# Performance work log

Measured on AMD Instinct MI355X. Metric: run time of the kernel, lower is better.

The kernel has to match this reference:

```python
import jax, jax.numpy as jnp
from jax import lax
import numpy as np

N, H, W, E, B = 4096, 7, 18, 16384, 64
NCONV = 3

def _conv2d(x, w, b=None):
    y = lax.conv_general_dilated(x, w, (1, 1), 'SAME', dimension_numbers=('NCHW', 'OIHW', 'NCHW'))
    return y if b is None else y + b[None, :, None, None]

def _bn(x, g, b):
    # training-mode batchnorm over (batch, H, W) per channel
    m = x.mean(axis=(0, 2, 3), keepdims=True)
    v = x.var(axis=(0, 2, 3), keepdims=True)
    return g[None, :, None, None] * (x - m) * lax.rsqrt(v + 1e-5) + b[None, :, None, None]

def _conv_layer(atom, es, et, nw, ew, lw, lb, bg, bb):
    # gather edge features (E,16,H,W); FastEdgeNetwork zip truncates to ONE iteration
    z = _conv2d(atom[et], ew)
    th = _conv2d(atom, nw)[es]
    z = jax.nn.elu(th * z)
    h = _conv2d(z, lw, lb)                      # (E,32,H,W)
    filt, core = jnp.split(h, 2, axis=1)
    msg = jax.nn.sigmoid(filt) * jax.nn.softplus(core)
    out = atom.at[es].add(msg)                  # scatter-add aggregation
    return atom + _bn(out, bg, bb)              # bn + residual


def setup_inputs() -> dict:
    key = jax.random.key(0)
    ks = iter(jax.random.split(key, 64))
    def rn(shape, s=0.05):
        return jax.random.normal(next(ks), shape, dtype=jnp.float32) * s
    d = {}
    d['nodes'] = jax.random.normal(next(ks), (N, H, W), dtype=jnp.float32)
    d['edge_sources'] = jax.random.randint(next(ks), (E,), 0, N)
    d['edge_targets'] = jax.random.randint(next(ks), (E,), 0, N)
    d['graph_indices'] = jnp.arange(N, dtype=jnp.int32) // (N // B)
    d['node_counts'] = jnp.full((B,), N // B, dtype=jnp.int32)
    d['nsites'] = jax.random.randint(next(ks), (B,), 1, 50)
    d['spacegroups'] = jax.random.randint(next(ks), (B,), 1, 231)
    d['emb_w'] = rn((16, 1, 3, 3)); d['emb_b'] = jnp.zeros((16,))
    d['cl_node_w'] = rn((NCONV, 16, 16, 3, 3)); d['cl_edge_w'] = rn((NCONV, 16, 16, 3, 3))
    d['cl_lin_w'] = rn((NCONV, 32, 16, 3, 3)); d['cl_lin_b'] = jnp.zeros((NCONV, 32))
    d['cl_bn_g'] = jnp.ones((NCONV, 16)); d['cl_bn_b'] = jnp.zeros((NCONV, 16))
    d['se_w1'] = rn((16, 2)); d['se_b1'] = jnp.zeros((16,))
    d['se_w2'] = rn((16, 2)); d['se_b2'] = jnp.zeros((16,))
    d['se_conv_w'] = rn((16, 1, 3, 3)); d['se_conv_b'] = jnp.zeros((16,))
    d['se_bn_g'] = jnp.ones((16,)); d['se_bn_b'] = jnp.zeros((16,))
    d['sf_conv_w'] = rn((16, 16, 3, 3)); d['sf_conv_b'] = jnp.zeros((16,))
    d['sf_bn_g'] = jnp.ones((16,)); d['sf_bn_b'] = jnp.zeros((16,))
    d['ctf_w'] = rn((16, 16, 3, 3)); d['ctf_b'] = jnp.zeros((16,))
    d['fc1_w'] = rn((32, 16 * H * W)); d['fc1_b'] = jnp.zeros((32,))
    d['fc2_w'] = rn((32, 32)); d['fc2_b'] = jnp.zeros((32,))
    d['reg_w'] = rn((1, 32)); d['reg_b'] = jnp.zeros((1,))
    d['fc3_w'] = rn((1, 144)); d['fc3_b'] = jnp.zeros((1,))
    d['eps'] = jnp.full((1,), 0.1, dtype=jnp.float32)
    return d


def reference(nodes, edge_sources, edge_targets, graph_indices, node_counts, nsites, spacegroups,
              emb_w, emb_b, cl_node_w, cl_edge_w, cl_lin_w, cl_lin_b, cl_bn_g, cl_bn_b,
              se_w1, se_b1, se_w2, se_b2, se_conv_w, se_conv_b, se_bn_g, se_bn_b,
              sf_conv_w, sf_conv_b, sf_bn_g, sf_bn_b, ctf_w, ctf_b,
              fc1_w, fc1_b, fc2_w, fc2_b, reg_w, reg_b, fc3_w, fc3_b, eps):
    sp = jax.nn.softplus
    # atom embedding: (N,1,7,18) -> (N,16,7,18)
    atom = sp(_conv2d(nodes[:, None], emb_w, emb_b))
    for l in range(NCONV):
        atom = _conv_layer(atom, edge_sources, edge_targets, cl_node_w[l], cl_edge_w[l],
                           cl_lin_w[l], cl_lin_b[l], cl_bn_g[l], cl_bn_b[l])
    # space branch: outer product of two 16-d embeddings of (nsites, spacegroup)
    so = jnp.stack([nsites, spacegroups], axis=1).astype(jnp.float32)    # (B,2)
    row = so @ se_w1.T + se_b1
    col = so @ se_w2.T + se_b2
    outer = (row[:, :, None] * col[:, None, :])[:, None]                 # (B,1,16,16)
    semb = sp(_bn(_conv2d(outer, se_conv_w, se_conv_b), se_bn_g, se_bn_b))  # (B,16,16,16)
    y = _bn(_conv2d(semb, sf_conv_w, sf_conv_b), sf_bn_g, sf_bn_b)
    y = lax.reduce_window(y, -jnp.inf, lax.max, (1, 1, 5, 5), (1, 1, 5, 5), 'VALID')  # (B,16,3,3)
    sflat = sp(y).reshape(B, -1)                                         # (B,144)
    # mean-pool atoms per crystal, conv_to_fc, MLP head
    crys = jax.ops.segment_sum(atom, graph_indices, num_segments=B)
    crys = crys / node_counts[:, None, None, None].astype(crys.dtype)    # (B,16,7,18)
    flat = sp(_conv2d(crys, ctf_w, ctf_b)).reshape(B, -1)                # (B,2016)
    h = sp(flat @ fc1_w.T + fc1_b)
    h = sp(h @ fc2_w.T + fc2_b)
    out = h @ reg_w.T + reg_b
    out = out + eps * (sflat @ fc3_w.T + fc3_b)                          # (B,1)
    return out
```

## Files before the change

### kernel.cpp

```cpp
#include <hip/hip_runtime.h>
#include <math.h>

#define HH 7
#define WW 18
#define PP 126
#define CC 16
#define NN 4096
#define EE 16384
#define BB 64
#define TILE 2016
#define ZT 2880

__device__ __forceinline__ float sp_f(float x) {
    return fmaxf(x, 0.f) + __logf(1.f + __expf(-fabsf(x)));
}
__device__ __forceinline__ float elu_f(float v) {
    return v > 0.f ? v : __expf(v) - 1.f;
}
__device__ __forceinline__ float sigm_f(float x) {
    return 1.f / (1.f + __expf(-x));
}

__global__ void k_wT_lin(const float* __restrict__ w, float* __restrict__ wT) {
    int i = blockIdx.x * 256 + threadIdx.x;
    if (i < 4608) {
        int q = i & 3, cb = (i >> 2) & 7, ci = (i >> 5) & 15, tap = i >> 9;
        int co = cb + ((q >> 1) & 1) * 8 + (q & 1) * 16;
        wT[i] = w[(co * 16 + ci) * 9 + tap];
    }
}
__global__ void k_wT_ne(const float* __restrict__ wN, const float* __restrict__ wE,
                        float* __restrict__ wT) {
    int i = blockIdx.x * 256 + threadIdx.x;
    if (i < 4608) {
        int q = i & 3, cb = (i >> 2) & 7, ci = (i >> 5) & 15, tap = i >> 9;
        int co = cb + ((q >> 1) & 1) * 8;
        const float* src = (q & 1) ? wE : wN;
        wT[i] = src[(co * 16 + ci) * 9 + tap];
    }
}

__global__ __launch_bounds__(256) void k_embed(const float* __restrict__ nodes,
                                               const float* __restrict__ w,
                                               const float* __restrict__ b,
                                               float* __restrict__ atom) {
    __shared__ float tile[PP];
    __shared__ float ws[CC * 9];
    __shared__ float bs[CC];
    int n = blockIdx.x, tid = threadIdx.x;
    for (int i = tid; i < PP; i += 256) tile[i] = nodes[n * PP + i];
    for (int i = tid; i < CC * 9; i += 256) ws[i] = w[i];
    if (tid < CC) bs[tid] = b[tid];
    __syncthreads();
    for (int i = tid; i < CC * PP; i += 256) {
        int c = i / PP, p = i - c * PP, y = p / WW, x = p - (p / WW) * WW;
        float acc = bs[c];
#pragma unroll
        for (int dy = 0; dy < 3; dy++) {
            int yy = y + dy - 1; if ((unsigned)yy >= (unsigned)HH) continue;
#pragma unroll
            for (int dx = 0; dx < 3; dx++) {
                int xx = x + dx - 1; if ((unsigned)xx >= (unsigned)WW) continue;
                acc += tile[yy * WW + xx] * ws[c * 9 + dy * 3 + dx];
            }
        }
        atom[(size_t)n * CC * PP + i] = sp_f(acc);
    }
}

__device__ __forceinline__ void conv_body4(const float* zt,
                                           const float (*ws)[16][8][4],
                                           int cb, int y,
                                           float* f0, float* c0,
                                           float* f1, float* c1) {
    for (int ci = 0; ci < 16; ci++) {
        const float* zb = zt + ci * 180 + y * 20;
#pragma unroll
        for (int dy = 0; dy < 3; dy++) {
            const float* zr = zb + dy * 20;
            float4 q0 = *(const float4*)&zr[0];
            float4 q1 = *(const float4*)&zr[4];
            float4 q2 = *(const float4*)&zr[8];
            float4 q3 = *(const float4*)&zr[12];
            float4 q4 = *(const float4*)&zr[16];
            float r[20];
            r[0]=q0.x; r[1]=q0.y; r[2]=q0.z; r[3]=q0.w;
            r[4]=q1.x; r[5]=q1.y; r[6]=q1.z; r[7]=q1.w;
            r[8]=q2.x; r[9]=q2.y; r[10]=q2.z; r[11]=q2.w;
            r[12]=q3.x; r[13]=q3.y; r[14]=q3.z; r[15]=q3.w;
            r[16]=q4.x; r[17]=q4.y; r[18]=q4.z; r[19]=q4.w;
            float4 w0 = *(const float4*)&ws[dy * 3 + 0][ci][cb][0];
            float4 w1 = *(const float4*)&ws[dy * 3 + 1][ci][cb][0];
            float4 w2 = *(const float4*)&ws[dy * 3 + 2][ci][cb][0];
#pragma unroll
            for (int x = 0; x < 18; x++) {
                f0[x] = fmaf(r[x],     w0.x, f0[x]);
                c0[x] = fmaf(r[x],     w0.y, c0[x]);
                f1[x] = fmaf(r[x],     w0.z, f1[x]);
                c1[x] = fmaf(r[x],     w0.w, c1[x]);
                f0[x] = fmaf(r[x + 1], w1.x, f0[x]);
                c0[x] = fmaf(r[x + 1], w1.y, c0[x]);
                f1[x] = fmaf(r[x + 1], w1.z, f1[x]);
                c1[x] = fmaf(r[x + 1], w1.w, c1[x]);
                f0[x] = fmaf(r[x + 2], w2.x, f0[x]);
                c0[x] = fmaf(r[x + 2], w2.y, c0[x]);
                f1[x] = fmaf(r[x + 2], w2.z, f1[x]);
                c1[x] = fmaf(r[x + 2], w2.w, c1[x]);
            }
        }
    }
}

__global__ __launch_bounds__(256) void k_node_conv2(const float* __restrict__ atom,
                                                    const float* __restrict__ wT,
                                                    float* __restrict__ An,
                                                    float* __restrict__ Ae) {
    __shared__ __align__(16) float zf[4 * ZT];
    __shared__ __align__(16) float ws4[9][16][8][4];
    int tid = threadIdx.x;
    for (int i = tid; i < 4608; i += 256) ((float*)ws4)[i] = wT[i];
    __syncthreads();

    int we = tid >> 6, lane = tid & 63;
    int n = blockIdx.x * 4 + we;
    float* zw = &zf[we * ZT];
    const float* src = atom + (size_t)n * TILE;
    for (int r = lane; r < ZT; r += 64) {
        int ci = r / 180, rr = r - ci * 180;
        int yy = rr / 20, xx = rr - yy * 20;
        float v = 0.f;
        if ((unsigned)(yy - 1) < 7u && (unsigned)(xx - 1) < 18u)
            v = src[ci * 126 + (yy - 1) * 18 + (xx - 1)];
        zw[r] = v;
    }
    int cb = lane & 7, y = lane >> 3;
    bool act = y < 7;
    float f0[18], c0[18], f1[18], c1[18];
#pragma unroll
    for (int x = 0; x < 18; x++) { f0[x] = 0.f; c0[x] = 0.f; f1[x] = 0.f; c1[x] = 0.f; }
    if (act) conv_body4(zw, ws4, cb, y, f0, c0, f1, c1);
    for (int r = lane; r < ZT; r += 64) zw[r] = 0.f;
    int b0 = cb * 180 + (y + 1) * 20 + 1;
    int b1 = (cb + 8) * 180 + (y + 1) * 20 + 1;
    if (act) {
#pragma unroll
        for (int x = 0; x < 18; x++) { zw[b0 + x] = f0[x]; zw[b1 + x] = f1[x]; }
    }
    float4* an4 = (float4*)&An[(size_t)n * ZT];
    for (int j = lane; j < ZT / 4; j += 64) an4[j] = ((const float4*)zw)[j];
    if (act) {
#pragma unroll
        for (int x = 0; x < 18; x++) { zw[b0 + x] = c0[x]; zw[b1 + x] = c1[x]; }
    }
    float4* ae4 = (float4*)&Ae[(size_t)n * ZT];
    for (int j = lane; j < ZT / 4; j += 64) ae4[j] = ((const float4*)zw)[j];
}

__global__ __launch_bounds__(256) void k_edge(const float* __restrict__ An,
                                              const float* __restrict__ Ae,
                                              const int* __restrict__ es,
                                              const int* __restrict__ et,
                                              const float* __restrict__ wT,
                                              const float* __restrict__ lb,
                                              float* __restrict__ outb) {
    __shared__ __align__(16) float zf[4 * ZT];
    __shared__ __align__(16) float ws4[9][16][8][4];
    int tid = threadIdx.x;
    for (int i = tid; i < 4608; i += 256) ((float*)ws4)[i] = wT[i];
    __syncthreads();

    int we = tid >> 6, lane = tid & 63;
    int e = blockIdx.x * 4 + we;
    int s = es[e], t = et[e];
    float* zw = &zf[we * ZT];
    const float4* an4 = (const float4*)&An[(size_t)s * ZT];
    const float4* ae4 = (const float4*)&Ae[(size_t)t * ZT];
    for (int j = lane; j < ZT / 4; j += 64) {
        float4 a4 = an4[j], b4 = ae4[j];
        float4 r;
        r.x = elu_f(a4.x * b4.x);
        r.y = elu_f(a4.y * b4.y);
        r.z = elu_f(a4.z * b4.z);
        r.w = elu_f(a4.w * b4.w);
        ((float4*)zw)[j] = r;
    }
    int cb = lane & 7, y = lane >> 3;
    bool act = y < 7;
    float f0[18], c0[18], f1[18], c1[18];
#pragma unroll
    for (int x = 0; x < 18; x++) { f0[x] = 0.f; c0[x] = 0.f; f1[x] = 0.f; c1[x] = 0.f; }
    if (act) conv_body4(zw, ws4, cb, y, f0, c0, f1, c1);
    if (act) {
        float bf0 = lb[cb], bc0 = lb[cb + 16], bf1 = lb[cb + 8], bc1 = lb[cb + 24];
        int base0 = cb * 126 + y * 18;
        int base1 = (cb + 8) * 126 + y * 18;
#pragma unroll
        for (int x = 0; x < 18; x++) {
            zw[base0 + x] = sigm_f(f0[x] + bf0) * sp_f(c0[x] + bc0);
            zw[base1 + x] = sigm_f(f1[x] + bf1) * sp_f(c1[x] + bc1);
        }
    }
    float* outn = outb + (size_t)s * TILE;
    for (int j = lane; j < TILE; j += 64)
        unsafeAtomicAdd(&outn[j], zw[j]);
}

template <int C, int S>
__global__ void k_bn_stats(const float* __restrict__ X, double* __restrict__ acc, int M) {
    int c = blockIdx.y, tid = threadIdx.x;
    double s1 = 0.0, s2 = 0.0;
    for (int m = blockIdx.x; m < M; m += gridDim.x) {
        const float* xr = &X[((size_t)m * C + c) * S];
        for (int s = tid; s < S; s += blockDim.x) {
            float v = xr[s];
            s1 += v; s2 += (double)v * v;
        }
    }
    __shared__ double sh1[256], sh2[256];
    sh1[tid] = s1; sh2[tid] = s2;
    __syncthreads();
    for (int off = blockDim.x >> 1; off > 0; off >>= 1) {
        if (tid < off) { sh1[tid] += sh1[tid + off]; sh2[tid] += sh2[tid + off]; }
        __syncthreads();
    }
    if (tid == 0) {
        unsafeAtomicAdd(&acc[2 * c], sh1[0]);
        unsafeAtomicAdd(&acc[2 * c + 1], sh2[0]);
    }
}

__global__ void k_bn_fin(const double* __restrict__ acc, const float* __restrict__ g,
                         const float* __restrict__ b, double invn,
                         float* __restrict__ scl, float* __restrict__ shf) {
    int c = threadIdx.x;
    if (c < 16) {
        double m = acc[2 * c] * invn;
        double v = acc[2 * c + 1] * invn - m * m;
        double s = (double)g[c] / sqrt(v + 1e-5);
        scl[c] = (float)s;
        shf[c] = (float)((double)b[c] - s * m);
    }
}

__global__ __launch_bounds__(256) void k_bn_res(float* __restrict__ atom,
                                                const float* __restrict__ outb,
                                                const float* __restrict__ scl,
                                                const float* __restrict__ shf) {
    __shared__ float sc[16], sh[16];
    int tid = threadIdx.x;
    if (tid < 16) { sc[tid] = scl[tid]; sh[tid] = shf[tid]; }
    __syncthreads();
    const long total = (long)NN * CC * PP;
    for (long i = (long)blockIdx.x * blockDim.x + tid; i < total;
         i += (long)gridDim.x * blockDim.x) {
        int c = (int)((i / PP) & 15);
        atom[i] += sc[c] * outb[i] + sh[c];
    }
}

__global__ __launch_bounds__(256) void k_pool(const float* __restrict__ atom,
                                              const int* __restrict__ gi,
                                              float* __restrict__ crys) {
    int n = blockIdx.x;
    int g = gi[n];
    const float* a = &atom[(size_t)n * CC * PP];
    float* cr = &crys[(size_t)g * CC * PP];
    for (int i = threadIdx.x; i < CC * PP; i += 256) unsafeAtomicAdd(&cr[i], a[i]);
}

__global__ __launch_bounds__(256) void k_ctf(const float* __restrict__ crys,
                                             const int* __restrict__ counts,
                                             const float* __restrict__ w,
                                             const float* __restrict__ b,
                                             float* __restrict__ flat) {
    __shared__ float tile[CC * PP];
    __shared__ float ws[CC * CC * 9];
    __shared__ float bs[CC];
    int g = blockIdx.x, tid = threadIdx.x;
    float cnt = (float)counts[g];
    for (int i = tid; i < CC * PP; i += 256) tile[i] = crys[(size_t)g * CC * PP + i] / cnt;
    for (int i = tid; i < CC * CC * 9; i += 256) ws[i] = w[i];
    if (tid < CC) bs[tid] = b[tid];
    __syncthreads();
    for (int i = tid; i < CC * PP; i += 256) {
        int co = i / PP, p = i - co * PP, y = p / WW, x = p - (p / WW) * WW;
        float acc = bs[co];
#pragma unroll
        for (int dy = 0; dy < 3; dy++) {
            int yy = y + dy - 1; if ((unsigned)yy >= (unsigned)HH) continue;
#pragma unroll
            for (int dx = 0; dx < 3; dx++) {
                int xx = x + dx - 1; if ((unsigned)xx >= (unsigned)WW) continue;
                int zoff = yy * WW + xx, tap = dy * 3 + dx;
                const float* tp = &tile[zoff];
                const float* wp = &ws[co * 144 + tap];
#pragma unroll
                for (int ci = 0; ci < CC; ci++) acc += tp[ci * PP] * wp[ci * 9];
            }
        }
        flat[(size_t)g * CC * PP + i] = sp_f(acc);
    }
}

__global__ __launch_bounds__(256) void k_space1(const int* __restrict__ nsites,
                                                const int* __restrict__ sgs,
                                                const float* __restrict__ w1,
                                                const float* __restrict__ b1,
                                                const float* __restrict__ w2,
                                                const float* __restrict__ b2,
                                                const float* __restrict__ cw,
                                                const float* __restrict__ cb,
                                                float* __restrict__ sembp) {
    __shared__ float outer[256];
    __shared__ float row[16], col[16];
    __shared__ float cws[144], cbs[16];
    int g = blockIdx.x, tid = threadIdx.x;
    if (tid < 16) {
        float ns = (float)nsites[g], sg = (float)sgs[g];
        row[tid] = ns * w1[2 * tid] + sg * w1[2 * tid + 1] + b1[tid];
        col[tid] = ns * w2[2 * tid] + sg * w2[2 * tid + 1] + b2[tid];
        cbs[tid] = cb[tid];
    }
    if (tid >= 64 && tid < 64 + 144) cws[tid - 64] = cw[tid - 64];
    __syncthreads();
    outer[tid] = row[tid >> 4] * col[tid & 15];
    __syncthreads();
    for (int i = tid; i < 16 * 256; i += 256) {
        int c = i >> 8, p = i & 255, y = p >> 4, x = p & 15;
        float acc = cbs[c];
#pragma unroll
        for (int dy = 0; dy < 3; dy++) {
            int yy = y + dy - 1; if ((unsigned)yy >= 16u) continue;
#pragma unroll
            for (int dx = 0; dx < 3; dx++) {
                int xx = x + dx - 1; if ((unsigned)xx >= 16u) continue;
                acc += outer[yy * 16 + xx] * cws[c * 9 + dy * 3 + dx];
            }
        }
        sembp[(size_t)g * 4096 + i] = acc;
    }
}

__global__ __launch_bounds__(256) void k_bn_sp256(const float* __restrict__ X,
                                                  float* __restrict__ Y,
                                                  const float* __restrict__ scl,
                                                  const float* __restrict__ shf) {
    __shared__ float sc[16], sh[16];
    if (threadIdx.x < 16) { sc[threadIdx.x] = scl[threadIdx.x]; sh[threadIdx.x] = shf[threadIdx.x]; }
    __syncthreads();
    int total = BB * 16 * 256;
    for (int i = blockIdx.x * blockDim.x + threadIdx.x; i < total;
         i += gridDim.x * blockDim.x) {
        int c = (i >> 8) & 15;
        Y[i] = sp_f(sc[c] * X[i] + sh[c]);
    }
}

__global__ __launch_bounds__(256) void k_space_conv(const float* __restrict__ X,
                                                    const float* __restrict__ w,
                                                    const float* __restrict__ b,
                                                    float* __restrict__ Y) {
    __shared__ float tile[16 * 256];
    __shared__ float ws[2304], bs[16];
    int g = blockIdx.x, tid = threadIdx.x;
    for (int i = tid; i < 4096; i += 256) tile[i] = X[(size_t)g * 4096 + i];
    for (int i = tid; i < 2304; i += 256) ws[i] = w[i];
    if (tid < 16) bs[tid] = b[tid];
    __syncthreads();
    for (int i = tid; i < 4096; i += 256) {
        int c = i >> 8, p = i & 255, y = p >> 4, x = p & 15;
        float acc = bs[c];
#pragma unroll
        for (int dy = 0; dy < 3; dy++) {
            int yy = y + dy - 1; if ((unsigned)yy >= 16u) continue;
#pragma unroll
            for (int dx = 0; dx < 3; dx++) {
                int xx = x + dx - 1; if ((unsigned)xx >= 16u) continue;
                int tap = dy * 3 + dx;
                const float* wp = &ws[c * 144 + tap];
                const float* tp = &tile[yy * 16 + xx];
#pragma unroll
                for (int ci = 0; ci < 16; ci++) acc += tp[ci * 256] * wp[ci * 9];
            }
        }
        Y[(size_t)g * 4096 + i] = acc;
    }
}

__global__ __launch_bounds__(256) void k_space_tail(const float* __restrict__ ypre,
                                                    const float* __restrict__ scl,
                                                    const float* __restrict__ shf,
                                                    const float* __restrict__ fc3w,
                                                    const float* __restrict__ fc3b,
                                                    float* __restrict__ sout) {
    __shared__ float red[256];
    int g = blockIdx.x, tid = threadIdx.x;
    float val = 0.f;
    if (tid < 144) {
        int c = tid / 9, cell = tid - c * 9, py = cell / 3, px = cell - py * 3;
        float sc = scl[c], sh = shf[c];
        float mx = -INFINITY;
        const float* base = &ypre[((size_t)g * 16 + c) * 256];
        for (int yy = py * 5; yy < py * 5 + 5; yy++)
            for (int xx = px * 5; xx < px * 5 + 5; xx++)
                mx = fmaxf(mx, sc * base[yy * 16 + xx] + sh);
        val = sp_f(mx) * fc3w[tid];
    }
    red[tid] = val;
    __syncthreads();
    for (int off = 128; off > 0; off >>= 1) {
        if (tid < off) red[tid] += red[tid + off];
        __syncthreads();
    }
    if (tid == 0) sout[g] = red[0] + fc3b[0];
}

__global__ __launch_bounds__(256) void k_head(const float* __restrict__ flat,
                                              const float* __restrict__ fc1w,
                                              const float* __restrict__ fc1b,
                                              const float* __restrict__ fc2w,
                                              const float* __restrict__ fc2b,
                                              const float* __restrict__ regw,
                                              const float* __restrict__ regb,
                                              const float* __restrict__ sout,
                                              const float* __restrict__ eps,
                                              float* __restrict__ out) {
    int g = blockIdx.x, tid = threadIdx.x;
    __shared__ float h1[32], h2[32];
    int o = tid >> 3, r = tid & 7;
    float part = 0.f;
    const float* fr = &flat[(size_t)g * 2016];
    const float* wr = &fc1w[(size_t)o * 2016];
    for (int j = r; j < 2016; j += 8) part += fr[j] * wr[j];
    part += __shfl_down(part, 4, 8);
    part += __shfl_down(part, 2, 8);
    part += __shfl_down(part, 1, 8);
    if (r == 0) h1[o] = sp_f(part + fc1b[o]);
    __syncthreads();
    if (tid < 32) {
        float a = fc2b[tid];
        for (int j = 0; j < 32; j++) a += h1[j] * fc2w[tid * 32 + j];
        h2[tid] = sp_f(a);
    }
    __syncthreads();
    if (tid == 0) {
        float a = regb[0];
        for (int j = 0; j < 32; j++) a += h2[j] * regw[j];
        out[g] = a + eps[0] * sout[g];
    }
}

extern "C" void kernel_launch(void* const* d_in, const int* in_sizes, int n_in,
                              void* d_out, int out_size, void* d_ws, size_t ws_size,
                              hipStream_t stream) {
    const float* nodes   = (const float*)d_in[0];
    const int*   es      = (const int*)d_in[1];
    const int*   et      = (const int*)d_in[2];
    const int*   gi      = (const int*)d_in[3];
    const int*   cnt     = (const int*)d_in[4];
    const int*   nsites  = (const int*)d_in[5];
    const int*   sgs     = (const int*)d_in[6];
    const float* emb_w   = (const float*)d_in[7];
    const float* emb_b   = (const float*)d_in[8];
    const float* cl_nw   = (const float*)d_in[9];
    const float* cl_ew   = (const float*)d_in[10];
    const float* cl_lw   = (const float*)d_in[11];
    const float* cl_lb   = (const float*)d_in[12];
    const float* cl_bg   = (const float*)d_in[13];
    const float* cl_bb   = (const float*)d_in[14];
    const float* se_w1   = (const float*)d_in[15];
    const float* se_b1   = (const float*)d_in[16];
    const float* se_w2   = (const float*)d_in[17];
    const float* se_b2   = (const float*)d_in[18];
    const float* se_cw   = (const float*)d_in[19];
    const float* se_cb   = (const float*)d_in[20];
    const float* se_bg   = (const float*)d_in[21];
    const float* se_bb   = (const float*)d_in[22];
    const float* sf_cw   = (const float*)d_in[23];
    const float* sf_cb   = (const float*)d_in[24];
    const float* sf_bg   = (const float*)d_in[25];
    const float* sf_bb   = (const float*)d_in[26];
    const float* ctf_w   = (const float*)d_in[27];
    const float* ctf_b   = (const float*)d_in[28];
    const float* fc1_w   = (const float*)d_in[29];
    const float* fc1_b   = (const float*)d_in[30];
    const float* fc2_w   = (const float*)d_in[31];
    const float* fc2_b   = (const float*)d_in[32];
    const float* reg_w   = (const float*)d_in[33];
    const float* reg_b   = (const float*)d_in[34];
    const float* fc3_w   = (const float*)d_in[35];
    const float* fc3_b   = (const float*)d_in[36];
    const float* eps     = (const float*)d_in[37];
    float* out = (float*)d_out;

    const size_t ATOM_B = (size_t)NN * TILE * sizeof(float);
    const size_t HALO_B = (size_t)NN * ZT * sizeof(float);
    char* ws = (char*)d_ws;
    float*  atom  = (float*)ws;              ws += ATOM_B;
    float*  An    = (float*)ws;              ws += HALO_B;
    float*  Ae    = (float*)ws;              ws += HALO_B;
    float*  outb  = (float*)ws;              ws += ATOM_B;
    double* acc   = (double*)ws;             ws += 256;
    float*  scl   = (float*)ws;              ws += 256;
    float*  shf   = (float*)ws;              ws += 256;
    float*  sout  = (float*)ws;              ws += 256;
    float*  nwT   = (float*)ws;              ws += 4608 * sizeof(float);
    float*  lwT   = (float*)ws;              ws += 4608 * sizeof(float);
    float*  crys  = (float*)ws;              ws += (size_t)BB * TILE * sizeof(float);
    float*  flat  = (float*)ws;              ws += (size_t)BB * TILE * sizeof(float);
    float*  sembp = (float*)ws;              ws += (size_t)BB * 16 * 256 * sizeof(float);
    float*  semb  = (float*)ws;              ws += (size_t)BB * 16 * 256 * sizeof(float);
    float*  ypre  = (float*)ws;              ws += (size_t)BB * 16 * 256 * sizeof(float);

    k_embed<<<NN, 256, 0, stream>>>(nodes, emb_w, emb_b, atom);

    for (int l = 0; l < 3; l++) {
        const float* nw = cl_nw + (size_t)l * CC * CC * 9;
        const float* ew = cl_ew + (size_t)l * CC * CC * 9;
        const float* lw = cl_lw + (size_t)l * 32 * CC * 9;
        const float* lb = cl_lb + (size_t)l * 32;
        const float* bg = cl_bg + (size_t)l * 16;
        const float* bb = cl_bb + (size_t)l * 16;

        k_wT_ne<<<18, 256, 0, stream>>>(nw, ew, nwT);
        k_wT_lin<<<18, 256, 0, stream>>>(lw, lwT);
        k_node_conv2<<<NN / 4, 256, 0, stream>>>(atom, nwT, An, Ae);
        hipMemcpyAsync(outb, atom, ATOM_B, hipMemcpyDeviceToDevice, stream);
        k_edge<<<EE / 4, 256, 0, stream>>>(An, Ae, es, et, lwT, lb, outb);
        hipMemsetAsync(acc, 0, 16 * 2 * sizeof(double), stream);
        k_bn_stats<16, 126><<<dim3(64, 16), 128, 0, stream>>>(outb, acc, NN);
        k_bn_fin<<<1, 16, 0, stream>>>(acc, bg, bb, 1.0 / ((double)NN * PP), scl, shf);
        k_bn_res<<<2048, 256, 0, stream>>>(atom, outb, scl, shf);
    }

    k_space1<<<BB, 256, 0, stream>>>(nsites, sgs, se_w1, se_b1, se_w2, se_b2,
                                     se_cw, se_cb, sembp);
    hipMemsetAsync(acc, 0, 16 * 2 * sizeof(double), stream);
    k_bn_stats<16, 256><<<dim3(8, 16), 256, 0, stream>>>(sembp, acc, BB);
    k_bn_fin<<<1, 16, 0, stream>>>(acc, se_bg, se_bb, 1.0 / (BB * 256.0), scl, shf);
    k_bn_sp256<<<256, 256, 0, stream>>>(sembp, semb, scl, shf);
    k_space_conv<<<BB, 256, 0, stream>>>(semb, sf_cw, sf_cb, ypre);
    hipMemsetAsync(acc, 0, 16 * 2 * sizeof(double), stream);
    k_bn_stats<16, 256><<<dim3(8, 16), 256, 0, stream>>>(ypre, acc, BB);
    k_bn_fin<<<1, 16, 0, stream>>>(acc, sf_bg, sf_bb, 1.0 / (BB * 256.0), scl, shf);
    k_space_tail<<<BB, 256, 0, stream>>>(ypre, scl, shf, fc3_w, fc3_b, sout);

    hipMemsetAsync(crys, 0, (size_t)BB * TILE * sizeof(float), stream);
    k_pool<<<NN, 256, 0, stream>>>(atom, gi, crys);
    k_ctf<<<BB, 256, 0, stream>>>(crys, cnt, ctf_w, ctf_b, flat);
    k_head<<<BB, 256, 0, stream>>>(flat, fc1_w, fc1_b, fc2_w, fc2_b,
                                   reg_w, reg_b, sout, eps, out);
}
```

Before: 1.465 ms.

## Halve per-wave shared staging buffer by processing input channels in two halves

The node-conv and edge kernels now stage only 8 input channels at a time in shared memory (1440 floats per wave instead of 2880), looping twice and accumulating into the same registers. The output write-back and atomic scatter are split into two halves that reuse the smaller buffer. This cuts LDS per block from roughly 64KB to about 41KB so more blocks can be resident per CU. The cost is extra phases of staging and write-back within each wave.

```diff
diff --git a/kernel.cpp b/kernel.cpp
--- a/kernel.cpp
+++ b/kernel.cpp
@@ -10,6 +10,7 @@
 #define BB 64
 #define TILE 2016
 #define ZT 2880
+#define ZTH 1440
 
 __device__ __forceinline__ float sp_f(float x) {
     return fmaxf(x, 0.f) + __logf(1.f + __expf(-fabsf(x)));
@@ -68,12 +69,12 @@
     }
 }
 
-__device__ __forceinline__ void conv_body4(const float* zt,
-                                           const float (*ws)[16][8][4],
-                                           int cb, int y,
-                                           float* f0, float* c0,
-                                           float* f1, float* c1) {
-    for (int ci = 0; ci < 16; ci++) {
+__device__ __forceinline__ void conv_body4h(const float* zt,
+                                            const float (*ws)[16][8][4],
+                                            int cih, int cb, int y,
+                                            float* f0, float* c0,
+                                            float* f1, float* c1) {
+    for (int ci = 0; ci < 8; ci++) {
         const float* zb = zt + ci * 180 + y * 20;
 #pragma unroll
         for (int dy = 0; dy < 3; dy++) {
@@ -89,9 +90,9 @@
             r[8]=q2.x; r[9]=q2.y; r[10]=q2.z; r[11]=q2.w;
             r[12]=q3.x; r[13]=q3.y; r[14]=q3.z; r[15]=q3.w;
             r[16]=q4.x; r[17]=q4.y; r[18]=q4.z; r[19]=q4.w;
-            float4 w0 = *(const float4*)&ws[dy * 3 + 0][ci][cb][0];
-            float4 w1 = *(const float4*)&ws[dy * 3 + 1][ci][cb][0];
-            float4 w2 = *(const float4*)&ws[dy * 3 + 2][ci][cb][0];
+            float4 w0 = *(const float4*)&ws[dy * 3 + 0][cih + ci][cb][0];
+            float4 w1 = *(const float4*)&ws[dy * 3 + 1][cih + ci][cb][0];
+            float4 w2 = *(const float4*)&ws[dy * 3 + 2][cih + ci][cb][0];
 #pragma unroll
             for (int x = 0; x < 18; x++) {
                 f0[x] = fmaf(r[x],     w0.x, f0[x]);
@@ -115,7 +116,7 @@
                                                     const float* __restrict__ wT,
                                                     float* __restrict__ An,
                                                     float* __restrict__ Ae) {
-    __shared__ __align__(16) float zf[4 * ZT];
+    __shared__ __align__(16) float zf[4 * ZTH];
     __shared__ __align__(16) float ws4[9][16][8][4];
     int tid = threadIdx.x;
     for (int i = tid; i < 4608; i += 256) ((float*)ws4)[i] = wT[i];
@@ -123,37 +124,49 @@
 
     int we = tid >> 6, lane = tid & 63;
     int n = blockIdx.x * 4 + we;
-    float* zw = &zf[we * ZT];
+    float* zw = &zf[we * ZTH];
     const float* src = atom + (size_t)n * TILE;
-    for (int r = lane; r < ZT; r += 64) {
-        int ci = r / 180, rr = r - ci * 180;
-        int yy = rr / 20, xx = rr - yy * 20;
-        float v = 0.f;
-        if ((unsigned)(yy - 1) < 7u && (unsigned)(xx - 1) < 18u)
-            v = src[ci * 126 + (yy - 1) * 18 + (xx - 1)];
-        zw[r] = v;
-    }
     int cb = lane & 7, y = lane >> 3;
     bool act = y < 7;
     float f0[18], c0[18], f1[18], c1[18];
 #pragma unroll
     for (int x = 0; x < 18; x++) { f0[x] = 0.f; c0[x] = 0.f; f1[x] = 0.f; c1[x] = 0.f; }
-    if (act) conv_body4(zw, ws4, cb, y, f0, c0, f1, c1);
-    for (int r = lane; r < ZT; r += 64) zw[r] = 0.f;
+#pragma unroll
+    for (int h = 0; h < 2; h++) {
+        for (int r = lane; r < ZTH; r += 64) {
+            int ci = r / 180, rr = r - ci * 180;
+            int yy = rr / 20, xx = rr - yy * 20;
+            float v = 0.f;
+            if ((unsigned)(yy - 1) < 7u && (unsigned)(xx - 1) < 18u)
+                v = src[(ci + 8 * h) * 126 + (yy - 1) * 18 + (xx - 1)];
+            zw[r] = v;
+        }
+        if (act) conv_body4h(zw, ws4, 8 * h, cb, y, f0, c0, f1, c1);
+    }
+    for (int r = lane; r < ZTH; r += 64) zw[r] = 0.f;
     int b0 = cb * 180 + (y + 1) * 20 + 1;
-    int b1 = (cb + 8) * 180 + (y + 1) * 20 + 1;
+    float4* an4 = (float4*)&An[(size_t)n * ZT];
+    float4* ae4 = (float4*)&Ae[(size_t)n * ZT];
     if (act) {
 #pragma unroll
-        for (int x = 0; x < 18; x++) { zw[b0 + x] = f0[x]; zw[b1 + x] = f1[x]; }
-    }
-    float4* an4 = (float4*)&An[(size_t)n * ZT];
-    for (int j = lane; j < ZT / 4; j += 64) an4[j] = ((const float4*)zw)[j];
+        for (int x = 0; x < 18; x++) zw[b0 + x] = f0[x];
+    }
+    for (int j = lane; j < ZTH / 4; j += 64) an4[j] = ((const float4*)zw)[j];
     if (act) {
 #pragma unroll
-        for (int x = 0; x < 18; x++) { zw[b0 + x] = c0[x]; zw[b1 + x] = c1[x]; }
-    }
-    float4* ae4 = (float4*)&Ae[(size_t)n * ZT];
-    for (int j = lane; j < ZT / 4; j += 64) ae4[j] = ((const float4*)zw)[j];
+        for (int x = 0; x < 18; x++) zw[b0 + x] = f1[x];
+    }
+    for (int j = lane; j < ZTH / 4; j += 64) an4[ZTH / 4 + j] = ((const float4*)zw)[j];
+    if (act) {
+#pragma unroll
+        for (int x = 0; x < 18; x++) zw[b0 + x] = c0[x];
+    }
+    for (int j = lane; j < ZTH / 4; j += 64) ae4[j] = ((const float4*)zw)[j];
+    if (act) {
+#pragma unroll
+        for (int x = 0; x < 18; x++) zw[b0 + x] = c1[x];
+    }
+    for (int j = lane; j < ZTH / 4; j += 64) ae4[ZTH / 4 + j] = ((const float4*)zw)[j];
 }
 
 __global__ __launch_bounds__(256) void k_edge(const float* __restrict__ An,
@@ -163,7 +176,7 @@
                                               const float* __restrict__ wT,
                                               const float* __restrict__ lb,
                                               float* __restrict__ outb) {
-    __shared__ __align__(16) float zf[4 * ZT];
+    __shared__ __align__(16) float zf[4 * ZTH];
     __shared__ __align__(16) float ws4[9][16][8][4];
     int tid = threadIdx.x;
     for (int i = tid; i < 4608; i += 256) ((float*)ws4)[i] = wT[i];
@@ -172,37 +185,45 @@
     int we = tid >> 6, lane = tid & 63;
     int e = blockIdx.x * 4 + we;
     int s = es[e], t = et[e];
-    float* zw = &zf[we * ZT];
-    const float4* an4 = (const float4*)&An[(size_t)s * ZT];
-    const float4* ae4 = (const float4*)&Ae[(size_t)t * ZT];
-    for (int j = lane; j < ZT / 4; j += 64) {
-        float4 a4 = an4[j], b4 = ae4[j];
-        float4 r;
-        r.x = elu_f(a4.x * b4.x);
-        r.y = elu_f(a4.y * b4.y);
-        r.z = elu_f(a4.z * b4.z);
-        r.w = elu_f(a4.w * b4.w);
-        ((float4*)zw)[j] = r;
-    }
+    float* zw = &zf[we * ZTH];
     int cb = lane & 7, y = lane >> 3;
     bool act = y < 7;
     float f0[18], c0[18], f1[18], c1[18];
 #pragma unroll
     for (int x = 0; x < 18; x++) { f0[x] = 0.f; c0[x] = 0.f; f1[x] = 0.f; c1[x] = 0.f; }
-    if (act) conv_body4(zw, ws4, cb, y, f0, c0, f1, c1);
+#pragma unroll
+    for (int h = 0; h < 2; h++) {
+        const float4* an4 = (const float4*)&An[(size_t)s * ZT + h * ZTH];
+        const float4* ae4 = (const float4*)&Ae[(size_t)t * ZT + h * ZTH];
+        for (int j = lane; j < ZTH / 4; j += 64) {
+            float4 a4 = an4[j], b4 = ae4[j];
+            float4 r;
+            r.x = elu_f(a4.x * b4.x);
+            r.y = elu_f(a4.y * b4.y);
+            r.z = elu_f(a4.z * b4.z);
+            r.w = elu_f(a4.w * b4.w);
+            ((float4*)zw)[j] = r;
+        }
+        if (act) conv_body4h(zw, ws4, 8 * h, cb, y, f0, c0, f1, c1);
+    }
+    float* outn = outb + (size_t)s * TILE;
+    int base = cb * 126 + y * 18;
     if (act) {
-        float bf0 = lb[cb], bc0 = lb[cb + 16], bf1 = lb[cb + 8], bc1 = lb[cb + 24];
-        int base0 = cb * 126 + y * 18;
-        int base1 = (cb + 8) * 126 + y * 18;
-#pragma unroll
-        for (int x = 0; x < 18; x++) {
-            zw[base0 + x] = sigm_f(f0[x] + bf0) * sp_f(c0[x] + bc0);
-            zw[base1 + x] = sigm_f(f1[x] + bf1) * sp_f(c1[x] + bc1);
-        }
-    }
-    float* outn = outb + (size_t)s * TILE;
-    for (int j = lane; j < TILE; j += 64)
+        float bf0 = lb[cb], bc0 = lb[cb + 16];
+#pragma unroll
+        for (int x = 0; x < 18; x++)
+            zw[base + x] = sigm_f(f0[x] + bf0) * sp_f(c0[x] + bc0);
+    }
+    for (int j = lane; j < 1008; j += 64)
         unsafeAtomicAdd(&outn[j], zw[j]);
+    if (act) {
+        float bf1 = lb[cb + 8], bc1 = lb[cb + 24];
+#pragma unroll
+        for (int x = 0; x < 18; x++)
+            zw[base + x] = sigm_f(f1[x] + bf1) * sp_f(c1[x] + bc1);
+    }
+    for (int j = lane; j < 1008; j += 64)
+        unsafeAtomicAdd(&outn[1008 + j], zw[j]);
 }
 
 template <int C, int S>
```

After: 1.537 ms. 1.05x slower.

## Use packed fp16 dot2 for the edge linear conv in k_edge

Applied to the files above, without the earlier changes.

The edge kernel now stores the ELU'd edge features in shared memory as packed fp16 pairs (channel c and c+8), and the lin-conv weights are pre-packed into fp16 pairs. The 3x3 conv uses v_dot2 (fdot2) with fp32 accumulation, which halves shared memory footprint and the number of inner-loop multiply-adds. The reduced LDS use may raise occupancy. The cost is lower precision for the conv inputs and weights, which could affect accuracy tolerance.

```diff
diff --git a/kernel.cpp b/kernel.cpp
--- a/kernel.cpp
+++ b/kernel.cpp
@@ -10,6 +10,17 @@
 #define BB 64
 #define TILE 2016
 #define ZT 2880
+#define EREG 2016
+
+typedef _Float16 h2 __attribute__((ext_vector_type(2)));
+
+#if __has_builtin(__builtin_amdgcn_fdot2)
+#define FDOT2(a, b, c) __builtin_amdgcn_fdot2((a), (b), (c), false)
+#else
+#define FDOT2(a, b, c) ((float)(a)[0] * (float)(b)[0] + ((float)(a)[1] * (float)(b)[1] + (c)))
+#endif
+
+__device__ __forceinline__ h2 bch2(float f) { return __builtin_bit_cast(h2, f); }
 
 __device__ __forceinline__ float sp_f(float x) {
     return fmaxf(x, 0.f) + __logf(1.f + __expf(-fabsf(x)));
@@ -21,14 +32,6 @@
     return 1.f / (1.f + __expf(-x));
 }
 
-__global__ void k_wT_lin(const float* __restrict__ w, float* __restrict__ wT) {
-    int i = blockIdx.x * 256 + threadIdx.x;
-    if (i < 4608) {
-        int q = i & 3, cb = (i >> 2) & 7, ci = (i >> 5) & 15, tap = i >> 9;
-        int co = cb + ((q >> 1) & 1) * 8 + (q & 1) * 16;
-        wT[i] = w[(co * 16 + ci) * 9 + tap];
-    }
-}
 __global__ void k_wT_ne(const float* __restrict__ wN, const float* __restrict__ wE,
                         float* __restrict__ wT) {
     int i = blockIdx.x * 256 + threadIdx.x;
@@ -37,6 +40,17 @@
         int co = cb + ((q >> 1) & 1) * 8;
         const float* src = (q & 1) ? wE : wN;
         wT[i] = src[(co * 16 + ci) * 9 + tap];
+    }
+}
+__global__ void k_wT_lin_h(const float* __restrict__ lw, unsigned int* __restrict__ wT) {
+    int i = blockIdx.x * 256 + threadIdx.x;
+    if (i < 2304) {
+        int q = i & 3, cb = (i >> 2) & 7, cp = (i >> 5) & 7, tap = i >> 8;
+        int co = cb + ((q >> 1) & 1) * 8 + (q & 1) * 16;
+        h2 v;
+        v[0] = (_Float16)lw[(co * 16 + cp) * 9 + tap];
+        v[1] = (_Float16)lw[(co * 16 + cp + 8) * 9 + tap];
+        wT[i] = __builtin_bit_cast(unsigned int, v);
     }
 }
 
@@ -160,49 +174,95 @@
                                               const float* __restrict__ Ae,
                                               const int* __restrict__ es,
                                               const int* __restrict__ et,
-                                              const float* __restrict__ wT,
+                                              const unsigned int* __restrict__ wTh,
                                               const float* __restrict__ lb,
                                               float* __restrict__ outb) {
-    __shared__ __align__(16) float zf[4 * ZT];
-    __shared__ __align__(16) float ws4[9][16][8][4];
+    __shared__ __align__(16) unsigned int zf[4 * EREG];
+    __shared__ __align__(16) unsigned int wsh[2304];
     int tid = threadIdx.x;
-    for (int i = tid; i < 4608; i += 256) ((float*)ws4)[i] = wT[i];
+    for (int i = tid; i < 2304; i += 256) wsh[i] = wTh[i];
     __syncthreads();
 
     int we = tid >> 6, lane = tid & 63;
     int e = blockIdx.x * 4 + we;
     int s = es[e], t = et[e];
-    float* zw = &zf[we * ZT];
-    const float4* an4 = (const float4*)&An[(size_t)s * ZT];
-    const float4* ae4 = (const float4*)&Ae[(size_t)t * ZT];
-    for (int j = lane; j < ZT / 4; j += 64) {
-        float4 a4 = an4[j], b4 = ae4[j];
-        float4 r;
-        r.x = elu_f(a4.x * b4.x);
-        r.y = elu_f(a4.y * b4.y);
-        r.z = elu_f(a4.z * b4.z);
-        r.w = elu_f(a4.w * b4.w);
-        ((float4*)zw)[j] = r;
+    unsigned int* zw = &zf[we * EREG];
+    const float4* anL = (const float4*)&An[(size_t)s * ZT];
+    const float4* aeL = (const float4*)&Ae[(size_t)t * ZT];
+    for (int j = lane; j < 360; j += 64) {
+        int cp = j / 45, p4 = j - cp * 45;
+        float4 al = anL[cp * 45 + p4];
+        float4 ah = anL[(cp + 8) * 45 + p4];
+        float4 bl = aeL[cp * 45 + p4];
+        float4 bh = aeL[(cp + 8) * 45 + p4];
+        float zl0 = elu_f(al.x * bl.x), zh0 = elu_f(ah.x * bh.x);
+        float zl1 = elu_f(al.y * bl.y), zh1 = elu_f(ah.y * bh.y);
+        float zl2 = elu_f(al.z * bl.z), zh2 = elu_f(ah.z * bh.z);
+        float zl3 = elu_f(al.w * bl.w), zh3 = elu_f(ah.w * bh.w);
+        uint4 o;
+        h2 p0; p0[0] = (_Float16)zl0; p0[1] = (_Float16)zh0; o.x = __builtin_bit_cast(unsigned int, p0);
+        h2 p1; p1[0] = (_Float16)zl1; p1[1] = (_Float16)zh1; o.y = __builtin_bit_cast(unsigned int, p1);
+        h2 p2; p2[0] = (_Float16)zl2; p2[1] = (_Float16)zh2; o.z = __builtin_bit_cast(unsigned int, p2);
+        h2 p3; p3[0] = (_Float16)zl3; p3[1] = (_Float16)zh3; o.w = __builtin_bit_cast(unsigned int, p3);
+        *(uint4*)&zw[cp * 180 + p4 * 4] = o;
     }
     int cb = lane & 7, y = lane >> 3;
     bool act = y < 7;
     float f0[18], c0[18], f1[18], c1[18];
 #pragma unroll
     for (int x = 0; x < 18; x++) { f0[x] = 0.f; c0[x] = 0.f; f1[x] = 0.f; c1[x] = 0.f; }
-    if (act) conv_body4(zw, ws4, cb, y, f0, c0, f1, c1);
+    if (act) {
+        const float4* wsf4 = (const float4*)wsh;
+        for (int cp = 0; cp < 8; cp++) {
+            const unsigned int* zb = zw + cp * 180 + y * 20;
+#pragma unroll
+            for (int dy = 0; dy < 3; dy++) {
+                const float4* zr4 = (const float4*)(zb + dy * 20);
+                float4 q0 = zr4[0], q1 = zr4[1], q2 = zr4[2], q3 = zr4[3], q4 = zr4[4];
+                h2 r[20];
+                r[0]=bch2(q0.x); r[1]=bch2(q0.y); r[2]=bch2(q0.z); r[3]=bch2(q0.w);
+                r[4]=bch2(q1.x); r[5]=bch2(q1.y); r[6]=bch2(q1.z); r[7]=bch2(q1.w);
+                r[8]=bch2(q2.x); r[9]=bch2(q2.y); r[10]=bch2(q2.z); r[11]=bch2(q2.w);
+                r[12]=bch2(q3.x); r[13]=bch2(q3.y); r[14]=bch2(q3.z); r[15]=bch2(q3.w);
+                r[16]=bch2(q4.x); r[17]=bch2(q4.y); r[18]=bch2(q4.z); r[19]=bch2(q4.w);
+                float4 w0f = wsf4[(dy * 3 + 0) * 64 + cp * 8 + cb];
+                float4 w1f = wsf4[(dy * 3 + 1) * 64 + cp * 8 + cb];
+                float4 w2f = wsf4[(dy * 3 + 2) * 64 + cp * 8 + cb];
+                h2 w0a = bch2(w0f.x), w0b = bch2(w0f.y), w0c = bch2(w0f.z), w0d = bch2(w0f.w);
+                h2 w1a = bch2(w1f.x), w1b = bch2(w1f.y), w1c = bch2(w1f.z), w1d = bch2(w1f.w);
+                h2 w2a = bch2(w2f.x), w2b = bch2(w2f.y), w2c = bch2(w2f.z), w2d = bch2(w2f.w);
+#pragma unroll
+                for (int x = 0; x < 18; x++) {
+                    f0[x] = FDOT2(r[x],     w0a, f0[x]);
+                    c0[x] = FDOT2(r[x],     w0b, c0[x]);
+                    f1[x] = FDOT2(r[x],     w0c, f1[x]);
+                    c1[x] = FDOT2(r[x],     w0d, c1[x]);
+                    f0[x] = FDOT2(r[x + 1], w1a, f0[x]);
+                    c0[x] = FDOT2(r[x + 1], w1b, c0[x]);
+                    f1[x] = FDOT2(r[x + 1], w1c, f1[x]);
+                    c1[x] = FDOT2(r[x + 1], w1d, c1[x]);
+                    f0[x] = FDOT2(r[x + 2], w2a, f0[x]);
+                    c0[x] = FDOT2(r[x + 2], w2b, c0[x]);
+                    f1[x] = FDOT2(r[x + 2], w2c, f1[x]);
+                    c1[x] = FDOT2(r[x + 2], w2d, c1[x]);
+                }
+            }
+        }
+    }
+    float* msgL = (float*)zw;
     if (act) {
         float bf0 = lb[cb], bc0 = lb[cb + 16], bf1 = lb[cb + 8], bc1 = lb[cb + 24];
         int base0 = cb * 126 + y * 18;
         int base1 = (cb + 8) * 126 + y * 18;
 #pragma unroll
         for (int x = 0; x < 18; x++) {
-            zw[base0 + x] = sigm_f(f0[x] + bf0) * sp_f(c0[x] + bc0);
-            zw[base1 + x] = sigm_f(f1[x] + bf1) * sp_f(c1[x] + bc1);
+            msgL[base0 + x] = sigm_f(f0[x] + bf0) * sp_f(c0[x] + bc0);
+            msgL[base1 + x] = sigm_f(f1[x] + bf1) * sp_f(c1[x] + bc1);
         }
     }
     float* outn = outb + (size_t)s * TILE;
     for (int j = lane; j < TILE; j += 64)
-        unsafeAtomicAdd(&outn[j], zw[j]);
+        unsafeAtomicAdd(&outn[j], msgL[j]);
 }
 
 template <int C, int S>
@@ -426,7 +486,7 @@
                                               const float* __restrict__ eps,
                                               float* __restrict__ out) {
     int g = blockIdx.x, tid = threadIdx.x;
-    __shared__ float h1[32], h2[32];
+    __shared__ float h1[32], h2s[32];
     int o = tid >> 3, r = tid & 7;
     float part = 0.f;
     const float* fr = &flat[(size_t)g * 2016];
@@ -440,12 +500,12 @@
     if (tid < 32) {
         float a = fc2b[tid];
         for (int j = 0; j < 32; j++) a += h1[j] * fc2w[tid * 32 + j];
-        h2[tid] = sp_f(a);
+        h2s[tid] = sp_f(a);
     }
     __syncthreads();
     if (tid == 0) {
         float a = regb[0];
-        for (int j = 0; j < 32; j++) a += h2[j] * regw[j];
+        for (int j = 0; j < 32; j++) a += h2s[j] * regw[j];
         out[g] = a + eps[0] * sout[g];
     }
 }
@@ -505,7 +565,7 @@
     float*  shf   = (float*)ws;              ws += 256;
     float*  sout  = (float*)ws;              ws += 256;
     float*  nwT   = (float*)ws;              ws += 4608 * sizeof(float);
-    float*  lwT   = (float*)ws;              ws += 4608 * sizeof(float);
+    unsigned int* lwTh = (unsigned int*)ws;  ws += 2304 * sizeof(unsigned int);
     float*  crys  = (float*)ws;              ws += (size_t)BB * TILE * sizeof(float);
     float*  flat  = (float*)ws;              ws += (size_t)BB * TILE * sizeof(float);
     float*  sembp = (float*)ws;              ws += (size_t)BB * 16 * 256 * sizeof(float);
@@ -523,10 +583,10 @@
         const float* bb = cl_bb + (size_t)l * 16;
 
         k_wT_ne<<<18, 256, 0, stream>>>(nw, ew, nwT);
-        k_wT_lin<<<18, 256, 0, stream>>>(lw, lwT);
+        k_wT_lin_h<<<9, 256, 0, stream>>>(lw, lwTh);
         k_node_conv2<<<NN / 4, 256, 0, stream>>>(atom, nwT, An, Ae);
         hipMemcpyAsync(outb, atom, ATOM_B, hipMemcpyDeviceToDevice, stream);
-        k_edge<<<EE / 4, 256, 0, stream>>>(An, Ae, es, et, lwT, lb, outb);
+        k_edge<<<EE / 4, 256, 0, stream>>>(An, Ae, es, et, lwTh, lb, outb);
         hipMemsetAsync(acc, 0, 16 * 2 * sizeof(double), stream);
         k_bn_stats<16, 126><<<dim3(64, 16), 128, 0, stream>>>(outb, acc, NN);
         k_bn_fin<<<1, 16, 0, stream>>>(acc, bg, bb, 1.0 / ((double)NN * PP), scl, shf);
```

New measurement: 1.341 ms. 1.09x faster.
